# Optimization experiments

Hardware: AMD Instinct MI355X
Metric: run time of the kernel (lower is better)

## Reference

```python
import jax, jax.numpy as jnp
import numpy as np

S, R, CM, H, CA, CZ = 128, 256, 256, 8, 32, 128


def _ln(x, w, b):
    mu = x.mean(-1, keepdims=True)
    var = x.var(-1, keepdims=True)
    return (x - mu) * jax.lax.rsqrt(var + 1e-5) * w + b


def setup_inputs() -> dict:
    key = jax.random.key(0)
    ks = jax.random.split(key, 20)
    n = lambda i, shape: jax.random.normal(ks[i], shape, jnp.float32) * 0.05
    return {
        "m": jax.random.normal(ks[0], (S, R, CM), jnp.float32),
        "m_mask": jnp.ones((S, R), jnp.float32),
        "z": jax.random.normal(ks[1], (R, R, CZ), jnp.float32),
        "row_ln_w": jnp.ones((CM,)), "row_ln_b": jnp.zeros((CM,)),
        "row_z_ln_w": jnp.ones((CZ,)), "row_z_ln_b": jnp.zeros((CZ,)),
        "row_wq": n(2, (CM, H * CA)), "row_wk": n(3, (CM, H * CA)), "row_wv": n(4, (CM, H * CA)),
        "row_wb": n(5, (CZ, H)),
        "row_wg": n(6, (CM, H * CA)), "row_bg": jnp.zeros((H * CA,)),
        "row_wo": n(7, (H * CA, CM)), "row_bo": jnp.zeros((CM,)),
        "col_ln_w": jnp.ones((CM,)), "col_ln_b": jnp.zeros((CM,)),
        "col_wq": n(8, (CM, H * CA)), "col_wk": n(9, (CM, H * CA)), "col_wv": n(10, (CM, H * CA)),
        "col_wg": n(11, (CM, H * CA)), "col_bg": jnp.zeros((H * CA,)),
        "col_wo": n(12, (H * CA, CM)), "col_bo": jnp.zeros((CM,)),
        "tr_ln_w": jnp.ones((CM,)), "tr_ln_b": jnp.zeros((CM,)),
        "tr_w1": n(13, (CM, 4 * CM)), "tr_b1": jnp.zeros((4 * CM,)),
        "tr_w2": n(14, (4 * CM, CM)), "tr_b2": jnp.zeros((CM,)),
    }


def _row_atten(m, m_mask, z, ln_w, ln_b, z_ln_w, z_ln_b, wq, wk, wv, wb, wg, bg, wo, bo):
    # MSA row attention with pair bias: attend over residues within each sequence row.
    x = _ln(m, ln_w, ln_b)                                   # [s,r,cm]
    q = (x @ wq).reshape(S, R, H, CA) * (CA ** -0.5)
    k = (x @ wk).reshape(S, R, H, CA)
    v = (x @ wv).reshape(S, R, H, CA)
    pair_bias = jnp.transpose(_ln(z, z_ln_w, z_ln_b) @ wb, (2, 0, 1))  # [h,r,r]
    mask_bias = (m_mask - 1.0)[:, None, None, :] * 1e9       # [s,1,1,r] over keys
    logits = jnp.einsum('sqhc,skhc->shqk', q, k) + pair_bias[None] + mask_bias
    a = jax.nn.softmax(logits, axis=-1)
    o = jnp.einsum('shqk,skhc->sqhc', a, v)
    g = jax.nn.sigmoid(x @ wg + bg).reshape(S, R, H, CA)
    return (g * o).reshape(S, R, H * CA) @ wo + bo


def _col_atten(m, m_mask, ln_w, ln_b, wq, wk, wv, wg, bg, wo, bo):
    # MSA column attention: attend over sequences within each residue column.
    x = _ln(m, ln_w, ln_b)                                   # [s,r,cm]
    q = (x @ wq).reshape(S, R, H, CA) * (CA ** -0.5)
    k = (x @ wk).reshape(S, R, H, CA)
    v = (x @ wv).reshape(S, R, H, CA)
    mask_bias = (jnp.transpose(m_mask) - 1.0)[:, None, None, :] * 1e9  # [r,1,1,s]
    logits = jnp.einsum('qrhc,krhc->rhqk', q, k) + mask_bias
    a = jax.nn.softmax(logits, axis=-1)
    o = jnp.einsum('rhqk,krhc->qrhc', a, v)
    g = jax.nn.sigmoid(x @ wg + bg).reshape(S, R, H, CA)
    return (g * o).reshape(S, R, H * CA) @ wo + bo


def _transition(m, ln_w, ln_b, w1, b1, w2, b2):
    x = _ln(m, ln_w, ln_b)
    return jax.nn.relu(x @ w1 + b1) @ w2 + b2


def reference(m, m_mask, z,
              row_ln_w, row_ln_b, row_z_ln_w, row_z_ln_b,
              row_wq, row_wk, row_wv, row_wb, row_wg, row_bg, row_wo, row_bo,
              col_ln_w, col_ln_b, col_wq, col_wk, col_wv, col_wg, col_bg, col_wo, col_bo,
              tr_ln_w, tr_ln_b, tr_w1, tr_b1, tr_w2, tr_b2):
    m = m + _row_atten(m, m_mask, z, row_ln_w, row_ln_b, row_z_ln_w, row_z_ln_b,
                       row_wq, row_wk, row_wv, row_wb, row_wg, row_bg, row_wo, row_bo)
    m = m + _col_atten(m, m_mask, col_ln_w, col_ln_b, col_wq, col_wk, col_wv,
                       col_wg, col_bg, col_wo, col_bo)
    m = m + _transition(m, tr_ln_w, tr_ln_b, tr_w1, tr_b1, tr_w2, tr_b2)
    return m
```

## Files before the change

### kernel.cpp

```cpp
#include <hip/hip_runtime.h>
#include <stdint.h>

#define S_ 128
#define R_ 256
#define CM_ 256
#define H_ 8
#define CA_ 32
#define CZ_ 128

typedef unsigned short u16;
typedef __bf16 bf16x8 __attribute__((ext_vector_type(8)));
typedef float f32x4 __attribute__((ext_vector_type(4)));

__device__ __forceinline__ float bf2f(u16 u){ unsigned v = ((unsigned)u) << 16; float f; __builtin_memcpy(&f, &v, 4); return f; }
__device__ __forceinline__ u16 f2bf(float f){ __bf16 h = (__bf16)f; u16 u; __builtin_memcpy(&u, &h, 2); return u; }
__device__ __forceinline__ unsigned pkbf(float lo, float hi){
  unsigned r; asm("v_cvt_pk_bf16_f32 %0, %1, %2" : "=v"(r) : "v"(lo), "v"(hi)); return r;
}

__device__ __forceinline__ void gl16(const void* g, void* l){
  __builtin_amdgcn_global_load_lds((const __attribute__((address_space(1))) void*)g,
                                   (__attribute__((address_space(3))) void*)l, 16, 0, 0);
}

struct WSrc { const float* p[12]; };
__global__ __launch_bounds__(256) void transpose_all(WSrc srcs, u16* __restrict__ dst){
  int b = blockIdx.x, t = threadIdx.x;
  int job, idx;
  if(b < 2560){ job = b >> 8; idx = ((b & 255) << 8) + t; }
  else if(b < 3584){ job = 10; idx = ((b - 2560) << 8) + t; }
  else { job = 11; idx = ((b - 3584) << 8) + t; }
  int K = (job == 11) ? 1024 : 256;
  int N = (job == 10) ? 1024 : 256;
  int off;
  if(job < 10) off = job * 65536;
  else if(job == 10) off = 655360;
  else off = 917504;
  int k = idx / N, n = idx - k * N;
  float sc = (job == 0 || job == 5) ? 0.17677669529663687f : 1.f;
  dst[off + n * K + k] = f2bf(srcs.p[job][idx] * sc);
}

__global__ __launch_bounds__(256) void ln_kernel(const float* __restrict__ in, const float* __restrict__ w,
                          const float* __restrict__ b, u16* __restrict__ out){
  int wv = threadIdx.x >> 6, lane = threadIdx.x & 63;
  long long row = (long long)blockIdx.x * 4 + wv;
  float4 v = ((const float4*)(in + row * CM_))[lane];
  float s = v.x + v.y + v.z + v.w;
  for(int mo = 32; mo; mo >>= 1) s += __shfl_xor(s, mo, 64);
  float mu = s * (1.f / CM_);
  float dx = v.x - mu, dy = v.y - mu, dz = v.z - mu, dw = v.w - mu;
  float s2 = dx * dx + dy * dy + dz * dz + dw * dw;
  for(int mo = 32; mo; mo >>= 1) s2 += __shfl_xor(s2, mo, 64);
  float rstd = rsqrtf(s2 * (1.f / CM_) + 1e-5f);
  float4 w4 = ((const float4*)w)[lane];
  float4 b4 = ((const float4*)b)[lane];
  ushort4 st;
  st.x = f2bf(dx * rstd * w4.x + b4.x);
  st.y = f2bf(dy * rstd * w4.y + b4.y);
  st.z = f2bf(dz * rstd * w4.z + b4.z);
  st.w = f2bf(dw * rstd * w4.w + b4.w);
  *(ushort4*)(out + row * CM_ + lane * 4) = st;
}

__global__ __launch_bounds__(256) void pair_bias_kernel(const float* __restrict__ z, const float* __restrict__ lnw,
                                 const float* __restrict__ lnb, const float* __restrict__ wb,
                                 u16* __restrict__ pb){
  int wv = threadIdx.x >> 6, lane = threadIdx.x & 63;
  long long row = (long long)blockIdx.x * 4 + wv;
  float2 v = ((const float2*)(z + row * CZ_))[lane];
  float s = v.x + v.y;
  for(int mo = 32; mo; mo >>= 1) s += __shfl_xor(s, mo, 64);
  float mu = s * (1.f / CZ_);
  float d0 = v.x - mu, d1 = v.y - mu;
  float s2 = d0 * d0 + d1 * d1;
  for(int mo = 32; mo; mo >>= 1) s2 += __shfl_xor(s2, mo, 64);
  float rstd = rsqrtf(s2 * (1.f / CZ_) + 1e-5f);
  float2 lw = ((const float2*)lnw)[lane], lb = ((const float2*)lnb)[lane];
  float x0 = d0 * rstd * lw.x + lb.x;
  float x1 = d1 * rstd * lw.y + lb.y;
  const float4* wp = (const float4*)(wb + lane * 16);
  float4 w0a = wp[0], w0b = wp[1], w1a = wp[2], w1b = wp[3];
  float acc[8];
  acc[0] = x0 * w0a.x + x1 * w1a.x; acc[1] = x0 * w0a.y + x1 * w1a.y;
  acc[2] = x0 * w0a.z + x1 * w1a.z; acc[3] = x0 * w0a.w + x1 * w1a.w;
  acc[4] = x0 * w0b.x + x1 * w1b.x; acc[5] = x0 * w0b.y + x1 * w1b.y;
  acc[6] = x0 * w0b.z + x1 * w1b.z; acc[7] = x0 * w0b.w + x1 * w1b.w;
  for(int mo = 32; mo; mo >>= 1){
    #pragma unroll
    for(int h = 0; h < 8; h++) acc[h] += __shfl_xor(acc[h], mo, 64);
  }
  if(lane < 8){
    int q = (int)(row >> 8), k = (int)(row & 255);
    int off = (((lane * 16 + (q >> 4)) * 16 + (k >> 4)) << 10)
            + ((((q >> 2) & 3) * 16 + (k & 15)) << 2) + (q & 3);
    pb[off] = f2bf(acc[lane]);
  }
}

template<bool HAS_BIAS, bool HAS_SIG, bool RELU, bool RES, bool F32OUT>
__global__ __launch_bounds__(256) void gemm128(
    const u16* __restrict__ A, const u16* __restrict__ Wt,
    const float* __restrict__ bias, const float* __restrict__ res,
    void* __restrict__ outv, int M, int N, int K, int sigStart){
  __shared__ __attribute__((aligned(16))) unsigned char Ab[16384];
  __shared__ __attribute__((aligned(16))) unsigned char Bb[16384];
  const int t = threadIdx.x;
  const int wv = t >> 6, lane = t & 63, l15 = lane & 15, l4 = lane >> 4;
  const int wm = wv >> 1, wn = wv & 1;
  const unsigned flat = blockIdx.y * gridDim.x + blockIdx.x;
  const unsigned NB = gridDim.x, mper = gridDim.y >> 3;
  const unsigned xcd = flat & 7, j = flat >> 3;
  const unsigned n_blk = j % NB, m_blk = xcd * mper + j / NB;
  const long long m0 = (long long)m_blk * 128;
  const int n0 = n_blk * 128;
  const int srow = t >> 3;
  const int ksw  = ((t & 7) ^ (srow & 7)) * 8;
  const u16* Ag = A  + (m0 + srow) * (long long)K + ksw;
  const u16* Bg = Wt + (long long)(n0 + srow) * K + ksw;
  f32x4 acc[4][4] = {};
  for(int kk = 0; kk < K; kk += 64){
    #pragma unroll
    for(int i = 0; i < 4; i++){
      gl16(Ag + (long long)i * 32 * K + kk, Ab + wv * 1024 + lane * 16 + i * 4096);
      gl16(Bg + (long long)i * 32 * K + kk, Bb + wv * 1024 + lane * 16 + i * 4096);
    }
    asm volatile("s_waitcnt vmcnt(0)" ::: "memory");
    __syncthreads();
    #pragma unroll
    for(int kh = 0; kh < 2; kh++){
      bf16x8 af[4], bq[4];
      #pragma unroll
      for(int mt = 0; mt < 4; mt++){
        int rr = wm * 64 + mt * 16 + l15;
        af[mt] = *(const bf16x8*)(Ab + rr * 128 + ((kh * 64 + l4 * 16) ^ ((rr & 7) << 4)));
      }
      #pragma unroll
      for(int nt = 0; nt < 4; nt++){
        int rr = wn * 64 + nt * 16 + l15;
        bq[nt] = *(const bf16x8*)(Bb + rr * 128 + ((kh * 64 + l4 * 16) ^ ((rr & 7) << 4)));
      }
      #pragma unroll
      for(int mt = 0; mt < 4; mt++)
        #pragma unroll
        for(int nt = 0; nt < 4; nt++)
          acc[mt][nt] = __builtin_amdgcn_mfma_f32_16x16x32_bf16(af[mt], bq[nt], acc[mt][nt], 0, 0, 0);
    }
    __syncthreads();
  }
  float bnt[4]; bool sg[4];
  #pragma unroll
  for(int nt = 0; nt < 4; nt++){
    int ncol = n0 + wn * 64 + nt * 16 + l15;
    bnt[nt] = 0.f; sg[nt] = false;
    if(HAS_BIAS){
      if(HAS_SIG){ sg[nt] = (ncol >= sigStart); bnt[nt] = sg[nt] ? bias[ncol - sigStart] : 0.f; }
      else bnt[nt] = bias[ncol];
    }
  }
  #pragma unroll
  for(int mt = 0; mt < 4; mt++){
    #pragma unroll
    for(int r = 0; r < 4; r++){
      long long mrow = m0 + wm * 64 + mt * 16 + l4 * 4 + r;
      #pragma unroll
      for(int nt = 0; nt < 4; nt++){
        int ncol = n0 + wn * 64 + nt * 16 + l15;
        float v = acc[mt][nt][r] + bnt[nt];
        if(HAS_SIG){ if(sg[nt]) v = 1.f / (1.f + __expf(-v)); }
        if(RELU) v = v > 0.f ? v : 0.f;
        if(RES)  v += res[mrow * N + ncol];
        if(F32OUT) ((float*)outv)[mrow * N + ncol] = v;
        else       ((u16*)outv)[mrow * N + ncol] = f2bf(v);
      }
    }
  }
}

template<int L, bool HAS_BIAS>
__global__ __launch_bounds__(256) void atten_kernel(
    const u16* __restrict__ qg, const u16* __restrict__ kg, const u16* __restrict__ vg,
    const u16* __restrict__ gg, const u16* __restrict__ pb, const float* __restrict__ mask,
    u16* __restrict__ og,
    long long obase_mul, long long tstride, long long obase_o, long long ostride,
    long long mbase_mul, int mstride){
  __shared__ __attribute__((aligned(16))) unsigned char smem[L * 128 + 8192];
  unsigned char* Kl = smem;
  unsigned char* Vt = smem + L * 64;
  unsigned char* Pl = smem + L * 128;

  const int t = threadIdx.x;
  const int wv = t >> 6, lane = t & 63, l15 = lane & 15, l4 = lane >> 4;
  const int h = blockIdx.x & 7;
  const int outer = blockIdx.x >> 3;
  const long long base  = (long long)outer * obase_mul + h * CA_;
  const long long baseo = (long long)outer * obase_o  + h * CA_;
  const long long mb = (long long)outer * mbase_mul;
  const int KT = L / 16, NC = L / 64;

  #pragma unroll
  for(int j = 0; j < L * 4; j += 256){
    int cid = j + t;
    int row = cid >> 2, ko = cid & 3;
    int4 kv = *(const int4*)(kg + base + (long long)row * tstride + ko * 8);
    *(int4*)(Kl + ((row * 64 + ko * 16) ^ ((row & 7) << 4))) = kv;
  }
  if(t < L){
    __attribute__((aligned(16))) u16 tmp[32];
    const u16* vp = vg + base + (long long)t * tstride;
    #pragma unroll
    for(int j2 = 0; j2 < 4; j2++) ((int4*)tmp)[j2] = *(const int4*)(vp + j2 * 8);
    int kp = (t >> 6) * 64 + (t & 15) * 4 + ((t >> 4) & 3);
    #pragma unroll
    for(int c = 0; c < 32; c++)
      *(u16*)(Vt + (((c * L + kp) * 2) ^ ((c & 7) << 4))) = tmp[c];
  }
  __syncthreads();

  float mskb[L / 16];
  #pragma unroll
  for(int kt = 0; kt < KT; kt++)
    mskb[kt] = (mask[mb + (long long)(kt * 16 + l15) * mstride] - 1.f) * 1e9f;

  unsigned char* Pw = Pl + wv * 2048;
  const int NQ = L / 4;
  #pragma unroll
  for(int qt = 0; qt < NQ / 16; qt++){
    const int qrow0 = wv * NQ + qt * 16;
    bf16x8 aq = *(const bf16x8*)(qg + base + (long long)(qrow0 + l15) * tstride + l4 * 8);
    f32x4 lac[L / 16];
    #pragma unroll
    for(int kt = 0; kt < KT; kt++){
      int kr = kt * 16 + l15;
      bf16x8 bk = *(const bf16x8*)(Kl + ((kr * 64 + l4 * 16) ^ ((kr & 7) << 4)));
      f32x4 zz = {0.f, 0.f, 0.f, 0.f};
      lac[kt] = __builtin_amdgcn_mfma_f32_16x16x32_bf16(aq, bk, zz, 0, 0, 0);
    }
    const u16* tile = HAS_BIAS ? (pb + (((h * 16 + (qrow0 >> 4)) * 16) << 10) + lane * 4) : nullptr;
    float sm[4] = {1e-30f, 1e-30f, 1e-30f, 1e-30f};
    #pragma unroll
    for(int kt = 0; kt < KT; kt++){
      float mm = mskb[kt];
      if(HAS_BIAS){
        ushort4 b4 = *(const ushort4*)(tile + (kt << 10));
        lac[kt][0] = __expf(lac[kt][0] + mm + bf2f(b4.x));
        lac[kt][1] = __expf(lac[kt][1] + mm + bf2f(b4.y));
        lac[kt][2] = __expf(lac[kt][2] + mm + bf2f(b4.z));
        lac[kt][3] = __expf(lac[kt][3] + mm + bf2f(b4.w));
      } else {
        #pragma unroll
        for(int r = 0; r < 4; r++) lac[kt][r] = __expf(lac[kt][r] + mm);
      }
      #pragma unroll
      for(int r = 0; r < 4; r++) sm[r] += lac[kt][r];
    }
    #pragma unroll
    for(int mo = 1; mo < 16; mo <<= 1)
      #pragma unroll
      for(int r = 0; r < 4; r++) sm[r] += __shfl_xor(sm[r], mo, 64);
    float inv[4];
    #pragma unroll
    for(int r = 0; r < 4; r++) inv[r] = 1.f / sm[r];
    f32x4 oac[2] = {{0,0,0,0},{0,0,0,0}};
    #pragma unroll
    for(int ch = 0; ch < NC; ch++){
      asm volatile("" ::: "memory");
      #pragma unroll
      for(int r = 0; r < 4; r++){
        int qp = l4 * 4 + r;
        uint2 pk2;
        pk2.x = pkbf(lac[ch * 4 + 0][r], lac[ch * 4 + 1][r]);
        pk2.y = pkbf(lac[ch * 4 + 2][r], lac[ch * 4 + 3][r]);
        *(uint2*)(Pw + qp * 128 + ((l15 * 8) ^ ((qp & 7) << 4))) = pk2;
      }
      asm volatile("s_waitcnt lgkmcnt(0)" ::: "memory");
      #pragma unroll
      for(int ksl = 0; ksl < 2; ksl++){
        bf16x8 ap = *(const bf16x8*)(Pw + l15 * 128 + ((ksl * 64 + l4 * 16) ^ ((l15 & 7) << 4)));
        #pragma unroll
        for(int ct = 0; ct < 2; ct++){
          int c = ct * 16 + l15;
          bf16x8 bv = *(const bf16x8*)(Vt + (((c * L + ch * 64 + ksl * 32 + l4 * 8) * 2) ^ ((c & 7) << 4)));
          oac[ct] = __builtin_amdgcn_mfma_f32_16x16x32_bf16(ap, bv, oac[ct], 0, 0, 0);
        }
      }
    }
    #pragma unroll
    for(int ct = 0; ct < 2; ct++)
      #pragma unroll
      for(int r = 0; r < 4; r++){
        int qi = qrow0 + l4 * 4 + r, c = ct * 16 + l15;
        float g = bf2f(gg[base + (long long)qi * tstride + c]);
        og[baseo + (long long)qi * ostride + c] = f2bf(oac[ct][r] * inv[r] * g);
      }
  }
}

extern "C" void kernel_launch(void* const* d_in, const int* in_sizes, int n_in,
                              void* d_out, int out_size, void* d_ws, size_t ws_size,
                              hipStream_t stream){
  const float* m        = (const float*)d_in[0];
  const float* m_mask   = (const float*)d_in[1];
  const float* z        = (const float*)d_in[2];
  const float* row_ln_w = (const float*)d_in[3];
  const float* row_ln_b = (const float*)d_in[4];
  const float* row_z_ln_w = (const float*)d_in[5];
  const float* row_z_ln_b = (const float*)d_in[6];
  const float* row_bg   = (const float*)d_in[12];
  const float* row_bo   = (const float*)d_in[14];
  const float* col_ln_w = (const float*)d_in[15];
  const float* col_ln_b = (const float*)d_in[16];
  const float* col_bg   = (const float*)d_in[21];
  const float* col_bo   = (const float*)d_in[23];
  const float* tr_ln_w  = (const float*)d_in[24];
  const float* tr_ln_b  = (const float*)d_in[25];
  const float* tr_b1    = (const float*)d_in[27];
  const float* tr_b2    = (const float*)d_in[29];
  float* out = (float*)d_out;
  char* ws = (char*)d_ws;

  u16* bx  = (u16*)ws;
  u16* fq  = bx + 8388608;
  u16* t_o = fq + 33554432;
  u16* pb  = t_o + 8388608;
  u16* wt  = pb + 2097152;

  WSrc srcs;
  srcs.p[0] = (const float*)d_in[7];
  srcs.p[1] = (const float*)d_in[8];
  srcs.p[2] = (const float*)d_in[9];
  srcs.p[3] = (const float*)d_in[11];
  srcs.p[4] = (const float*)d_in[13];
  srcs.p[5] = (const float*)d_in[17];
  srcs.p[6] = (const float*)d_in[18];
  srcs.p[7] = (const float*)d_in[19];
  srcs.p[8] = (const float*)d_in[20];
  srcs.p[9] = (const float*)d_in[22];
  srcs.p[10] = (const float*)d_in[26];
  srcs.p[11] = (const float*)d_in[28];

  dim3 b256(256);
  transpose_all<<<dim3(4608), b256, 0, stream>>>(srcs, wt);
  pair_bias_kernel<<<dim3(16384), b256, 0, stream>>>(z, row_z_ln_w, row_z_ln_b,
                                                     (const float*)d_in[10], pb);

  ln_kernel<<<dim3(8192), b256, 0, stream>>>(m, row_ln_w, row_ln_b, bx);
  gemm128<true,true,false,false,false><<<dim3(8,256), b256, 0, stream>>>(
      bx, wt, row_bg, nullptr, fq, 32768, 1024, 256, 768);
  atten_kernel<256,true><<<dim3(1024), b256, 0, stream>>>(
      fq, fq + 256, fq + 512, fq + 768, pb, m_mask, t_o,
      262144, 1024, 65536, 256, 256, 1);
  gemm128<true,false,false,true,true><<<dim3(2,256), b256, 0, stream>>>(
      t_o, wt + 262144, row_bo, m, out, 32768, 256, 256, 0);

  ln_kernel<<<dim3(8192), b256, 0, stream>>>(out, col_ln_w, col_ln_b, bx);
  gemm128<true,true,false,false,false><<<dim3(8,256), b256, 0, stream>>>(
      bx, wt + 327680, col_bg, nullptr, fq, 32768, 1024, 256, 768);
  atten_kernel<128,false><<<dim3(2048), b256, 0, stream>>>(
      fq, fq + 256, fq + 512, fq + 768, nullptr, m_mask, t_o,
      1024, 262144, 256, 65536, 1, 256);
  gemm128<true,false,false,true,true><<<dim3(2,256), b256, 0, stream>>>(
      t_o, wt + 589824, col_bo, out, out, 32768, 256, 256, 0);

  ln_kernel<<<dim3(8192), b256, 0, stream>>>(out, tr_ln_w, tr_ln_b, bx);
  gemm128<true,false,true,false,false><<<dim3(8,256), b256, 0, stream>>>(
      bx, wt + 655360, tr_b1, nullptr, fq, 32768, 1024, 256, 0);
  gemm128<true,false,false,true,true><<<dim3(2,256), b256, 0, stream>>>(
      fq, wt + 917504, tr_b2, out, out, 32768, 256, 1024, 0);
}
```

Measured before the change: 314.7 us.

## Compute pair bias with MFMA over 32-row tiles instead of shuffle reductions

The pair-bias kernel now handles 32 rows of z per block. Each row's layernorm is spread over 8 lanes, and the normalized rows are packed to bf16 in swizzled LDS along with a zero-padded bf16 copy of wb. A 16x16x32 bf16 MFMA then produces the 8 head projections, replacing the wave-wide shuffle reductions over 8 accumulators per row. The aim is to cut shuffle traffic and block count, at the cost of bf16 rounding of the normalized z and wb before the projection, and half the waves sit idle during the MFMA phase.

```diff
diff --git a/kernel.cpp b/kernel.cpp
--- a/kernel.cpp
+++ b/kernel.cpp
@@ -66,35 +66,80 @@
 __global__ __launch_bounds__(256) void pair_bias_kernel(const float* __restrict__ z, const float* __restrict__ lnw,
                                  const float* __restrict__ lnb, const float* __restrict__ wb,
                                  u16* __restrict__ pb){
-  int wv = threadIdx.x >> 6, lane = threadIdx.x & 63;
-  long long row = (long long)blockIdx.x * 4 + wv;
-  float2 v = ((const float2*)(z + row * CZ_))[lane];
-  float s = v.x + v.y;
-  for(int mo = 32; mo; mo >>= 1) s += __shfl_xor(s, mo, 64);
-  float mu = s * (1.f / CZ_);
-  float d0 = v.x - mu, d1 = v.y - mu;
-  float s2 = d0 * d0 + d1 * d1;
-  for(int mo = 32; mo; mo >>= 1) s2 += __shfl_xor(s2, mo, 64);
-  float rstd = rsqrtf(s2 * (1.f / CZ_) + 1e-5f);
-  float2 lw = ((const float2*)lnw)[lane], lb = ((const float2*)lnb)[lane];
-  float x0 = d0 * rstd * lw.x + lb.x;
-  float x1 = d1 * rstd * lw.y + lb.y;
-  const float4* wp = (const float4*)(wb + lane * 16);
-  float4 w0a = wp[0], w0b = wp[1], w1a = wp[2], w1b = wp[3];
-  float acc[8];
-  acc[0] = x0 * w0a.x + x1 * w1a.x; acc[1] = x0 * w0a.y + x1 * w1a.y;
-  acc[2] = x0 * w0a.z + x1 * w1a.z; acc[3] = x0 * w0a.w + x1 * w1a.w;
-  acc[4] = x0 * w0b.x + x1 * w1b.x; acc[5] = x0 * w0b.y + x1 * w1b.y;
-  acc[6] = x0 * w0b.z + x1 * w1b.z; acc[7] = x0 * w0b.w + x1 * w1b.w;
-  for(int mo = 32; mo; mo >>= 1){
-    #pragma unroll
-    for(int h = 0; h < 8; h++) acc[h] += __shfl_xor(acc[h], mo, 64);
-  }
-  if(lane < 8){
-    int q = (int)(row >> 8), k = (int)(row & 255);
-    int off = (((lane * 16 + (q >> 4)) * 16 + (k >> 4)) << 10)
-            + ((((q >> 2) & 3) * 16 + (k & 15)) << 2) + (q & 3);
-    pb[off] = f2bf(acc[lane]);
+  __shared__ __attribute__((aligned(16))) unsigned char Xl[32 * 256];
+  __shared__ __attribute__((aligned(16))) unsigned char Wl[16 * 256];
+  const int t = threadIdx.x;
+  const int wv = t >> 6, lane = t & 63, l15 = lane & 15, l4 = lane >> 4;
+  const int r0 = blockIdx.x * 32;
+
+  if(t < 128){
+    const float4* wr = (const float4*)(wb + t * 8);
+    float4 a = wr[0], bq = wr[1];
+    u16 vals[8] = {f2bf(a.x), f2bf(a.y), f2bf(a.z), f2bf(a.w),
+                   f2bf(bq.x), f2bf(bq.y), f2bf(bq.z), f2bf(bq.w)};
+    #pragma unroll
+    for(int n = 0; n < 8; n++){
+      *(u16*)(Wl + ((n * 256 + t * 2) ^ ((n & 7) << 4))) = vals[n];
+      *(u16*)(Wl + (((n + 8) * 256 + t * 2) ^ ((n & 7) << 4))) = 0;
+    }
+  }
+  {
+    int row = wv * 8 + (lane >> 3);
+    int c0 = (lane & 7) * 16;
+    const float4* rp = (const float4*)(z + (long long)(r0 + row) * CZ_ + c0);
+    float4 v0 = rp[0], v1 = rp[1], v2 = rp[2], v3 = rp[3];
+    float s = v0.x + v0.y + v0.z + v0.w + v1.x + v1.y + v1.z + v1.w
+            + v2.x + v2.y + v2.z + v2.w + v3.x + v3.y + v3.z + v3.w;
+    s += __shfl_xor(s, 1, 64); s += __shfl_xor(s, 2, 64); s += __shfl_xor(s, 4, 64);
+    float mu = s * (1.f / CZ_);
+    float d[16] = {v0.x - mu, v0.y - mu, v0.z - mu, v0.w - mu,
+                   v1.x - mu, v1.y - mu, v1.z - mu, v1.w - mu,
+                   v2.x - mu, v2.y - mu, v2.z - mu, v2.w - mu,
+                   v3.x - mu, v3.y - mu, v3.z - mu, v3.w - mu};
+    float s2 = 0.f;
+    #pragma unroll
+    for(int i = 0; i < 16; i++) s2 += d[i] * d[i];
+    s2 += __shfl_xor(s2, 1, 64); s2 += __shfl_xor(s2, 2, 64); s2 += __shfl_xor(s2, 4, 64);
+    float rstd = rsqrtf(s2 * (1.f / CZ_) + 1e-5f);
+    const float4* wp = (const float4*)(lnw + c0);
+    const float4* bp = (const float4*)(lnb + c0);
+    float x[16];
+    #pragma unroll
+    for(int i = 0; i < 4; i++){
+      float4 w4 = wp[i], b4 = bp[i];
+      x[i * 4 + 0] = d[i * 4 + 0] * rstd * w4.x + b4.x;
+      x[i * 4 + 1] = d[i * 4 + 1] * rstd * w4.y + b4.y;
+      x[i * 4 + 2] = d[i * 4 + 2] * rstd * w4.z + b4.z;
+      x[i * 4 + 3] = d[i * 4 + 3] * rstd * w4.w + b4.w;
+    }
+    uint4 p0, p1;
+    p0.x = pkbf(x[0], x[1]);  p0.y = pkbf(x[2], x[3]);
+    p0.z = pkbf(x[4], x[5]);  p0.w = pkbf(x[6], x[7]);
+    p1.x = pkbf(x[8], x[9]);  p1.y = pkbf(x[10], x[11]);
+    p1.z = pkbf(x[12], x[13]); p1.w = pkbf(x[14], x[15]);
+    *(uint4*)(Xl + ((row * 256 + c0 * 2) ^ ((row & 7) << 4))) = p0;
+    *(uint4*)(Xl + ((row * 256 + c0 * 2 + 16) ^ ((row & 7) << 4))) = p1;
+  }
+  __syncthreads();
+  if(wv < 2){
+    f32x4 acc = {0.f, 0.f, 0.f, 0.f};
+    #pragma unroll
+    for(int ks = 0; ks < 4; ks++){
+      int rowA = wv * 16 + l15;
+      bf16x8 a = *(const bf16x8*)(Xl + ((rowA * 256 + l4 * 16 + ks * 64) ^ ((rowA & 7) << 4)));
+      bf16x8 b = *(const bf16x8*)(Wl + ((l15 * 256 + l4 * 16 + ks * 64) ^ ((l15 & 7) << 4)));
+      acc = __builtin_amdgcn_mfma_f32_16x16x32_bf16(a, b, acc, 0, 0, 0);
+    }
+    if(l15 < 8){
+      #pragma unroll
+      for(int r = 0; r < 4; r++){
+        int rowg = r0 + wv * 16 + l4 * 4 + r;
+        int q = rowg >> 8, k = rowg & 255;
+        int off = (((l15 * 16 + (q >> 4)) * 16 + (k >> 4)) << 10)
+                + ((((q >> 2) & 3) * 16 + (k & 15)) << 2) + (q & 3);
+        pb[off] = f2bf(acc[r]);
+      }
+    }
   }
 }
 
@@ -341,8 +386,8 @@
 
   dim3 b256(256);
   transpose_all<<<dim3(4608), b256, 0, stream>>>(srcs, wt);
-  pair_bias_kernel<<<dim3(16384), b256, 0, stream>>>(z, row_z_ln_w, row_z_ln_b,
-                                                     (const float*)d_in[10], pb);
+  pair_bias_kernel<<<dim3(2048), b256, 0, stream>>>(z, row_z_ln_w, row_z_ln_b,
+                                                    (const float*)d_in[10], pb);
 
   ln_kernel<<<dim3(8192), b256, 0, stream>>>(m, row_ln_w, row_ln_b, bx);
   gemm128<true,true,false,false,false><<<dim3(8,256), b256, 0, stream>>>(
```

Result: faster. 283.5 us (-9.9%).
